# Optimization experiments

Measured on AMD Instinct MI355X. Metric: run time of the kernel, lower is better.

The kernel has to match this reference:

```python
import jax, jax.numpy as jnp
import numpy as np

B, H, OUT, L_LAYERS = 64, 1024, 512, 2
SEQ = 256
SOS_VALUE = -2.0  # predict_binary_output=False


def setup_inputs() -> dict:
    key = jax.random.key(0)
    ks = jax.random.split(key, 16)
    s_ih0 = 1.0 / np.sqrt(OUT)
    s_h = 1.0 / np.sqrt(H)
    return {
        "encoder_output": jax.random.normal(ks[0], (B, SEQ, OUT), jnp.float32),
        "h0": jax.random.normal(ks[1], (L_LAYERS, B, H), jnp.float32),
        "c0": jax.random.normal(ks[2], (L_LAYERS, B, H), jnp.float32),
        "W_ih0": jax.random.normal(ks[3], (4 * H, OUT), jnp.float32) * s_ih0,
        "W_hh0": jax.random.normal(ks[4], (4 * H, H), jnp.float32) * s_h,
        "b_ih0": jax.random.normal(ks[5], (4 * H,), jnp.float32) * s_h,
        "b_hh0": jax.random.normal(ks[6], (4 * H,), jnp.float32) * s_h,
        "W_ih1": jax.random.normal(ks[7], (4 * H, H), jnp.float32) * s_h,
        "W_hh1": jax.random.normal(ks[8], (4 * H, H), jnp.float32) * s_h,
        "b_ih1": jax.random.normal(ks[9], (4 * H,), jnp.float32) * s_h,
        "b_hh1": jax.random.normal(ks[10], (4 * H,), jnp.float32) * s_h,
        "W_fc": jax.random.normal(ks[11], (OUT, H), jnp.float32) * s_h,
        "b_fc": jax.random.normal(ks[12], (OUT,), jnp.float32) * s_h,
        "seq_length": SEQ,
    }


def _lstm_cell(x, h, c, Wih, Whh, bih, bhh):
    # PyTorch gate order: i, f, g, o
    gates = x @ Wih.T + h @ Whh.T + (bih + bhh)
    i, f, g, o = jnp.split(gates, 4, axis=-1)
    i = jax.nn.sigmoid(i)
    f = jax.nn.sigmoid(f)
    g = jnp.tanh(g)
    o = jax.nn.sigmoid(o)
    c_new = f * c + i * g
    h_new = o * jnp.tanh(c_new)
    return h_new, c_new


def reference(encoder_output, h0, c0, W_ih0, W_hh0, b_ih0, b_hh0,
              W_ih1, W_hh1, b_ih1, b_hh1, W_fc, b_fc, seq_length):
    batch = h0.shape[1]
    y_init = jnp.full((batch, OUT), SOS_VALUE, dtype=h0.dtype)  # SOS token
    layers = ((W_ih0, W_hh0, b_ih0, b_hh0), (W_ih1, W_hh1, b_ih1, b_hh1))

    def step(carry, _):
        h, c, y = carry  # h, c: (num_layers, B, H); y: (B, OUT)
        x = y
        hs, cs = [], []
        for l, (Wih, Whh, bih, bhh) in enumerate(layers):
            h_l, c_l = _lstm_cell(x, h[l], c[l], Wih, Whh, bih, bhh)
            hs.append(h_l)
            cs.append(c_l)
            x = h_l
        y_hat = jax.nn.relu(x @ W_fc.T + b_fc)
        return (jnp.stack(hs), jnp.stack(cs), y_hat), y_hat

    (_, _, _), ys = jax.lax.scan(step, (h0, c0, y_init), None, length=seq_length)
    return jnp.transpose(ys, (1, 0, 2))  # (B, seq_length, OUT)
```

## Files before the change

kernel.cpp:

```cpp
#include <hip/hip_runtime.h>
#include <stdint.h>


#define NBLK 256
#define NTHR 256
#define HDIM 1024
#define ODIM 512
#define BDIM 64
#define SEQL 256
#define LEAD0 224

typedef _Float16 v8h __attribute__((ext_vector_type(8)));
typedef float    v4f __attribute__((ext_vector_type(4)));

#define WL0_NS 48
#define WL1_NS 64
#define WFC_NS 32
#define WL0_OFF 0
#define WL1_OFF (WL0_NS*1024)
#define WFC_OFF (WL1_OFF + WL1_NS*1024)
#define SMEM_BYTES (WFC_OFF + WFC_NS*1024)

#define YB_SZ  (BDIM*ODIM*2)
#define HB_SZ  (BDIM*HDIM*2)

#define FH0_REL 0
#define FH1_REL (4*256*4)
#define FY_REL  (FH1_REL + 4*256*4)
#define EH0_REL (FY_REL + 4*32*4)
#define EY_REL  (EH0_REL + 4*8*64)
#define FLG_BYTES (EY_REL + 4*8*64)

__device__ __forceinline__ float fsig(float x)   { return 1.0f / (1.0f + __expf(-x)); }
__device__ __forceinline__ float ftanhf(float x) { return 1.0f - 2.0f / (__expf(2.0f*x) + 1.0f); }

__device__ __forceinline__ unsigned long long ald8(const void* p){
  return __hip_atomic_load((const unsigned long long*)p, __ATOMIC_RELAXED, __HIP_MEMORY_SCOPE_AGENT);
}
__device__ __forceinline__ unsigned int ald4(const void* p){
  return __hip_atomic_load((const unsigned int*)p, __ATOMIC_RELAXED, __HIP_MEMORY_SCOPE_AGENT);
}
__device__ __forceinline__ void ast4(void* p, unsigned int v){
  __hip_atomic_store((unsigned int*)p, v, __ATOMIC_RELAXED, __HIP_MEMORY_SCOPE_AGENT);
}

__device__ __forceinline__ void wrap_inv(){
  asm volatile("s_waitcnt vmcnt(0)\n\tbuffer_inv sc1" ::: "memory");
}

__device__ __forceinline__ void wait_word(const unsigned int* w, unsigned int tag){
  while (ald4(w) < tag) __builtin_amdgcn_s_sleep(1);
  asm volatile("" ::: "memory");
}

__device__ __forceinline__ void scan256_pub(const unsigned int* rowf, unsigned int* ew,
                                            unsigned int tag){
  const char* p = (const char*)(rowf + (threadIdx.x & 63)*4);
  while (true){
    unsigned long long a = ald8(p);
    unsigned long long b = ald8(p+8);
    unsigned int m0 = (unsigned int)a, m1 = (unsigned int)(a >> 32);
    unsigned int m2 = (unsigned int)b, m3 = (unsigned int)(b >> 32);
    unsigned int m = min(min(m0, m1), min(m2, m3));
    if (__all(m >= tag)) break;
    __builtin_amdgcn_s_sleep(1);
  }
  if ((threadIdx.x & 63) == 0) ast4(ew, tag);
  asm volatile("" ::: "memory");
}

__device__ __forceinline__ void scan32_pub(const unsigned int* rowf, unsigned int* ew,
                                           unsigned int tag){
  const unsigned int* p = rowf + (threadIdx.x & 31);
  while (!__all(ald4(p) >= tag)) __builtin_amdgcn_s_sleep(1);
  if ((threadIdx.x & 63) == 0) ast4(ew, tag);
  asm volatile("" ::: "memory");
}

__device__ __forceinline__ void wait_grp256(const unsigned int* rowf, unsigned int tag){
  const char* p = (const char*)(rowf + (threadIdx.x & 63)*4);
  while (true){
    unsigned long long a = ald8(p);
    unsigned long long b = ald8(p+8);
    unsigned int m0 = (unsigned int)a, m1 = (unsigned int)(a >> 32);
    unsigned int m2 = (unsigned int)b, m3 = (unsigned int)(b >> 32);
    unsigned int m = min(min(m0, m1), min(m2, m3));
    if (__all(m >= tag)) break;
    __builtin_amdgcn_s_sleep(1);
  }
  asm volatile("" ::: "memory");
}

__device__ __forceinline__ void publish(unsigned int* flag, unsigned int tag){
  asm volatile("s_waitcnt vmcnt(0)" ::: "memory");
  if ((threadIdx.x & 63) == 0) ast4(flag, tag);
}

template<int NC>
__device__ __forceinline__ v4f gemm_phase(const char* const cb[], const char* wl, v4f acc){
  v8h A[4][8];
  constexpr int PF = (NC < 3) ? NC : 3;
  #pragma unroll
  for (int p = 0; p < PF; p++){
    #pragma unroll
    for (int j = 0; j < 8; j++) A[p][j] = *(const v8h*)(cb[p] + (size_t)j*64);
  }
  #pragma unroll
  for (int c = 0; c < NC; c++){
    const int cur = c & 3, nx = (c + 3) & 3;
    if (c + 3 < NC){
      #pragma unroll
      for (int j = 0; j < 8; j++) A[nx][j] = *(const v8h*)(cb[c+3] + (size_t)j*64);
    }
    #pragma unroll
    for (int j = 0; j < 8; j++){
      v8h B = *(const v8h*)(wl + (size_t)(c*8 + j)*1024);
      acc = __builtin_amdgcn_mfma_f32_16x16x32_f16(A[cur][j], B, acc, 0, 0, 0);
    }
  }
  return acc;
}

__device__ __forceinline__ void gemm_dual4(const char* const cb[], const char* wlA,
                                           const char* wlB, v4f& accA, v4f& accB){
  v8h A[4][8];
  #pragma unroll
  for (int p = 0; p < 3; p++){
    #pragma unroll
    for (int j = 0; j < 8; j++) A[p][j] = *(const v8h*)(cb[p] + (size_t)j*64);
  }
  #pragma unroll
  for (int c = 0; c < 4; c++){
    const int cur = c & 3, nx = (c + 3) & 3;
    if (c + 3 < 4){
      #pragma unroll
      for (int j = 0; j < 8; j++) A[nx][j] = *(const v8h*)(cb[c+3] + (size_t)j*64);
    }
    #pragma unroll
    for (int j = 0; j < 8; j++){
      v8h BA = *(const v8h*)(wlA + (size_t)(c*8 + j)*1024);
      accA = __builtin_amdgcn_mfma_f32_16x16x32_f16(A[cur][j], BA, accA, 0, 0, 0);
      v8h BB = *(const v8h*)(wlB + (size_t)(c*8 + j)*1024);
      accB = __builtin_amdgcn_mfma_f32_16x16x32_f16(A[cur][j], BB, accB, 0, 0, 0);
    }
  }
}

__device__ __forceinline__ void lstm_epi_pack(v4f acc, float bias, float* cs,
                                              char* hbase, int l15, int gidx){
  #pragma unroll
  for (int r = 0; r < 4; r++){
    float v  = acc[r] + bias;
    float x1 = __shfl_xor(v, 1);
    float x2 = __shfl_xor(v, 2);
    float x3 = __shfl_xor(v, 3);
    float vi = (gidx==0)?v :(gidx==1)?x1:(gidx==2)?x2:x3;
    float vf = (gidx==1)?v :(gidx==0)?x1:(gidx==3)?x2:x3;
    float vg = (gidx==2)?v :(gidx==3)?x1:(gidx==0)?x2:x3;
    float vo = (gidx==3)?v :(gidx==2)?x1:(gidx==1)?x2:x3;
    float ii = fsig(vi), ff = fsig(vf), gg = ftanhf(vg), oo = fsig(vo);
    float cn = ff*cs[r] + ii*gg;
    cs[r] = cn;
    float hn = oo * ftanhf(cn);
    unsigned int uv = (unsigned int)__builtin_bit_cast(unsigned short, (_Float16)hn);
    unsigned int o4 = (unsigned int)__shfl_xor((int)uv, 4);
    unsigned int pr = uv | (o4 << 16);
    unsigned int o8 = (unsigned int)__shfl_xor((int)pr, 8);
    if (l15 == 0){
      unsigned long long full = (unsigned long long)pr | ((unsigned long long)o8 << 32);
      __hip_atomic_store((unsigned long long*)(hbase + (size_t)r*(HDIM*2)), full,
                         __ATOMIC_RELAXED, __HIP_MEMORY_SCOPE_AGENT);
    }
  }
}

__global__ void init_kernel(const float* __restrict__ h0,
                            _Float16* __restrict__ h0bi, _Float16* __restrict__ h1bi,
                            _Float16* __restrict__ ybi){
  int i = blockIdx.x*256 + threadIdx.x;
  if (i < BDIM*HDIM){
    h0bi[i] = (_Float16)h0[i];
    h1bi[i] = (_Float16)h0[BDIM*HDIM + i];
  }
  if (i < BDIM*ODIM) ybi[i] = (_Float16)(-2.0f);
}

__launch_bounds__(NTHR, 1)
__global__ void decoder_kernel(
    const float* __restrict__ Wih0, const float* __restrict__ Whh0,
    const float* __restrict__ bih0, const float* __restrict__ bhh0,
    const float* __restrict__ Wih1, const float* __restrict__ Whh1,
    const float* __restrict__ bih1, const float* __restrict__ bhh1,
    const float* __restrict__ Wfc,  const float* __restrict__ bfc,
    const float* __restrict__ c0in, float* __restrict__ out,
    char* __restrict__ yB, char* __restrict__ h0B, char* __restrict__ h1B,
    char* __restrict__ flg, int dmask)
{
  extern __shared__ char smem[];
  const int bid = blockIdx.x;
  const int tid = threadIdx.x;
  const int wv  = tid >> 6;
  const int ln  = tid & 63;
  const int l15 = ln & 15;
  const int lq  = ln >> 4;
  const int u0  = bid * 4;
  const int f   = bid & 7;
  const int leader = (bid >= LEAD0 && bid < LEAD0 + 8);

  unsigned int* fh0r = (unsigned int*)(flg + FH0_REL) + wv*256;
  unsigned int* fh1r = (unsigned int*)(flg + FH1_REL) + wv*256;
  unsigned int* fyr  = (unsigned int*)(flg + FY_REL)  + wv*32;
  unsigned int* eh0  = (unsigned int*)(flg + EH0_REL + (wv*8 + f)*64);
  unsigned int* ey   = (unsigned int*)(flg + EY_REL  + (wv*8 + f)*64);

  for (int slot = tid; slot < WL0_NS*64; slot += NTHR){
    int s = slot >> 6, l = slot & 63;
    int r16 = l & 15, q = l >> 4;
    int grow = (r16 & 3)*HDIM + u0 + (r16 >> 2);
    int kb = s*32 + q*8;
    const float* src; int k0;
    if (kb < ODIM){ src = Wih0 + (size_t)grow*ODIM; k0 = kb; }
    else          { src = Whh0 + (size_t)grow*HDIM; k0 = kb - ODIM; }
    v8h hv;
    #pragma unroll
    for (int j = 0; j < 8; j++) hv[j] = (_Float16)src[k0 + j];
    *(v8h*)(smem + WL0_OFF + s*1024 + l*16) = hv;
  }
  for (int slot = tid; slot < WL1_NS*64; slot += NTHR){
    int s = slot >> 6, l = slot & 63;
    int r16 = l & 15, q = l >> 4;
    int grow = (r16 & 3)*HDIM + u0 + (r16 >> 2);
    int kb = s*32 + q*8;
    const float* src; int k0;
    if (kb < HDIM){ src = Wih1 + (size_t)grow*HDIM; k0 = kb; }
    else          { src = Whh1 + (size_t)grow*HDIM; k0 = kb - HDIM; }
    v8h hv;
    #pragma unroll
    for (int j = 0; j < 8; j++) hv[j] = (_Float16)src[k0 + j];
    *(v8h*)(smem + WL1_OFF + s*1024 + l*16) = hv;
  }
  if (bid < 32){
    for (int slot = tid; slot < WFC_NS*64; slot += NTHR){
      int s = slot >> 6, l = slot & 63;
      int r16 = l & 15, q = l >> 4;
      const float* src = Wfc + (size_t)(bid*16 + r16)*HDIM;
      int k0 = s*32 + q*8;
      v8h hv;
      #pragma unroll
      for (int j = 0; j < 8; j++) hv[j] = (_Float16)src[k0 + j];
      *(v8h*)(smem + WFC_OFF + s*1024 + l*16) = hv;
    }
  }
  __syncthreads();

  const int gidx = l15 & 3;
  const int unit = u0 + (l15 >> 2);
  const int growL = gidx*HDIM + unit;
  const float bias0 = bih0[growL] + bhh0[growL];
  const float bias1 = bih1[growL] + bhh1[growL];
  float biasf = 0.f;
  if (bid < 32) biasf = bfc[bid*16 + l15];

  const int rb = wv*16 + lq*4;
  float cs0[4], cs1[4];
  #pragma unroll
  for (int r = 0; r < 4; r++){
    int b = rb + r;
    cs0[r] = c0in[(size_t)(0*BDIM + b)*HDIM + unit];
    cs1[r] = c0in[(size_t)(1*BDIM + b)*HDIM + unit];
  }

  const int row = wv*16 + l15;
  const size_t aoffY = (size_t)row*ODIM*2 + (size_t)lq*16;
  const size_t aoffH = (size_t)row*HDIM*2 + (size_t)lq*16;
  const size_t hwoff = ((size_t)rb*HDIM + u0)*2;
  const char* wl0 = smem + WL0_OFF + ln*16;
  const char* wl1 = smem + WL1_OFF + ln*16;
  const char* wlf = smem + WFC_OFF + ln*16;
  const char* wl0r = wl0 + 16*1024;
  const char* wl1r = wl1 + 32*1024;

  v4f p0 = {0.f,0.f,0.f,0.f};
  {
    const char* hi = h0B + (size_t)dmask*HB_SZ + aoffH;
    const char* cb[4] = { hi, hi+512, hi+1024, hi+1536 };
    p0 = gemm_phase<4>(cb, wl0r, p0);
  }

  for (int t = 0; t < SEQL; t++){
    const int sp = (t - 1) & dmask;
    const int sc = t & dmask;

    if ((t & dmask) == 0) wrap_inv();

    if (t > 0){
      if (leader) scan32_pub(fyr, ey, (unsigned)t);
      else        wait_word(ey, (unsigned)t);
    }

    {
      const char* ysrc = yB + (size_t)sp*YB_SZ + aoffY;
      const char* cb[2] = { ysrc, ysrc+512 };
      v4f acc = gemm_phase<2>(cb, wl0, p0);
      lstm_epi_pack(acc, bias0, cs0, h0B + (size_t)sc*HB_SZ + hwoff, l15, gidx);
    }
    publish(&fh0r[bid], (unsigned)(t+1));

    v4f p1 = {0.f,0.f,0.f,0.f};
    {
      const char* hs = h1B + (size_t)sp*HB_SZ + aoffH;
      const char* cb[4] = { hs, hs+512, hs+1024, hs+1536 };
      if (leader){
        scan256_pub(fh0r, eh0, (unsigned)(t+1));
        p1 = gemm_phase<4>(cb, wl1r, p1);
      } else {
        p1 = gemm_phase<4>(cb, wl1r, p1);
        wait_word(eh0, (unsigned)(t+1));
      }
    }

    {
      const char* hs = h0B + (size_t)sc*HB_SZ + aoffH;
      const char* cb[4] = { hs, hs+512, hs+1024, hs+1536 };
      v4f np0 = {0.f,0.f,0.f,0.f};
      gemm_dual4(cb, wl1, wl0r, p1, np0);
      lstm_epi_pack(p1, bias1, cs1, h1B + (size_t)sc*HB_SZ + hwoff, l15, gidx);
      p0 = np0;
    }
    publish(&fh1r[bid], (unsigned)(t+1));

    if (bid < 32){
      wait_grp256(fh1r, (unsigned)(t+1));
      const char* f1 = h1B + (size_t)sc*HB_SZ + aoffH;
      const char* cb[4] = { f1, f1+512, f1+1024, f1+1536 };
      v4f acc = {0.f,0.f,0.f,0.f};
      acc = gemm_phase<4>(cb, wlf, acc);
      char* ydst = yB + (size_t)sc*YB_SZ;
      float yv[4];
      #pragma unroll
      for (int r = 0; r < 4; r++){
        float v = fmaxf(acc[r] + biasf, 0.f);
        yv[r] = v;
        unsigned int uv = (unsigned int)__builtin_bit_cast(unsigned short, (_Float16)v);
        unsigned int o1 = (unsigned int)__shfl_xor((int)uv, 1);
        unsigned int pr = uv | (o1 << 16);
        unsigned int o2 = (unsigned int)__shfl_xor((int)pr, 2);
        if ((l15 & 3) == 0){
          int b = rb + r;
          int o = bid*16 + l15;
          unsigned long long full = (unsigned long long)pr | ((unsigned long long)o2 << 32);
          __hip_atomic_store((unsigned long long*)(ydst + ((size_t)b*ODIM + o)*2),
                             full, __ATOMIC_RELAXED, __HIP_MEMORY_SCOPE_AGENT);
        }
      }
      publish(&fyr[bid], (unsigned)(t+1));
      #pragma unroll
      for (int r = 0; r < 4; r++){
        int b = rb + r;
        int o = bid*16 + l15;
        out[((size_t)b*SEQL + t)*ODIM + o] = yv[r];
      }
    }
  }
}

extern "C" void kernel_launch(void* const* d_in, const int* in_sizes, int n_in,
                              void* d_out, int out_size, void* d_ws, size_t ws_size,
                              hipStream_t stream){
  (void)in_sizes; (void)n_in; (void)out_size;

  int D = 16;
  while (D > 2 && (size_t)D*(YB_SZ + 2*HB_SZ) + FLG_BYTES > ws_size) D >>= 1;
  if ((size_t)D*(YB_SZ + 2*HB_SZ) + FLG_BYTES > ws_size) return;

  char* ws  = (char*)d_ws;
  char* yB  = ws;
  char* h0B = yB + (size_t)D*YB_SZ;
  char* h1B = h0B + (size_t)D*HB_SZ;
  char* flg = h1B + (size_t)D*HB_SZ;

  const float* h0   = (const float*)d_in[1];
  const float* c0   = (const float*)d_in[2];
  const float* Wih0 = (const float*)d_in[3];
  const float* Whh0 = (const float*)d_in[4];
  const float* bih0 = (const float*)d_in[5];
  const float* bhh0 = (const float*)d_in[6];
  const float* Wih1 = (const float*)d_in[7];
  const float* Whh1 = (const float*)d_in[8];
  const float* bih1 = (const float*)d_in[9];
  const float* bhh1 = (const float*)d_in[10];
  const float* Wfc  = (const float*)d_in[11];
  const float* bfc  = (const float*)d_in[12];
  float* out = (float*)d_out;

  (void)hipMemsetAsync(flg, 0, FLG_BYTES, stream);
  hipLaunchKernelGGL(init_kernel, dim3(256), dim3(256), 0, stream,
                     h0,
                     (_Float16*)(h0B + (size_t)(D-1)*HB_SZ),
                     (_Float16*)(h1B + (size_t)(D-1)*HB_SZ),
                     (_Float16*)(yB  + (size_t)(D-1)*YB_SZ));

  (void)hipFuncSetAttribute((const void*)decoder_kernel,
                            hipFuncAttributeMaxDynamicSharedMemorySize, SMEM_BYTES);
  hipLaunchKernelGGL(decoder_kernel, dim3(NBLK), dim3(NTHR), SMEM_BYTES, stream,
                     Wih0, Whh0, bih0, bhh0, Wih1, Whh1, bih1, bhh1,
                     Wfc, bfc, c0, out, yB, h0B, h1B, flg, D - 1);
}
```

Measured before the change: 5.753 ms.

## Spread FC output projection across all blocks and split sync leaders per stage

```diff
diff --git a/kernel.cpp b/kernel.cpp
--- a/kernel.cpp
+++ b/kernel.cpp
@@ -8,7 +8,6 @@
 #define ODIM 512
 #define BDIM 64
 #define SEQL 256
-#define LEAD0 224
 
 typedef _Float16 v8h __attribute__((ext_vector_type(8)));
 typedef float    v4f __attribute__((ext_vector_type(4)));
@@ -27,8 +26,9 @@
 #define FH0_REL 0
 #define FH1_REL (4*256*4)
 #define FY_REL  (FH1_REL + 4*256*4)
-#define EH0_REL (FY_REL + 4*32*4)
-#define EY_REL  (EH0_REL + 4*8*64)
+#define EH0_REL (FY_REL + 4*256*4)
+#define EH1_REL (EH0_REL + 4*8*64)
+#define EY_REL  (EH1_REL + 4*8*64)
 #define FLG_BYTES (EY_REL + 4*8*64)
 
 __device__ __forceinline__ float fsig(float x)   { return 1.0f / (1.0f + __expf(-x)); }
@@ -66,28 +66,6 @@
     __builtin_amdgcn_s_sleep(1);
   }
   if ((threadIdx.x & 63) == 0) ast4(ew, tag);
-  asm volatile("" ::: "memory");
-}
-
-__device__ __forceinline__ void scan32_pub(const unsigned int* rowf, unsigned int* ew,
-                                           unsigned int tag){
-  const unsigned int* p = rowf + (threadIdx.x & 31);
-  while (!__all(ald4(p) >= tag)) __builtin_amdgcn_s_sleep(1);
-  if ((threadIdx.x & 63) == 0) ast4(ew, tag);
-  asm volatile("" ::: "memory");
-}
-
-__device__ __forceinline__ void wait_grp256(const unsigned int* rowf, unsigned int tag){
-  const char* p = (const char*)(rowf + (threadIdx.x & 63)*4);
-  while (true){
-    unsigned long long a = ald8(p);
-    unsigned long long b = ald8(p+8);
-    unsigned int m0 = (unsigned int)a, m1 = (unsigned int)(a >> 32);
-    unsigned int m2 = (unsigned int)b, m3 = (unsigned int)(b >> 32);
-    unsigned int m = min(min(m0, m1), min(m2, m3));
-    if (__all(m >= tag)) break;
-    __builtin_amdgcn_s_sleep(1);
-  }
   asm volatile("" ::: "memory");
 }
 
@@ -205,12 +183,15 @@
   const int lq  = ln >> 4;
   const int u0  = bid * 4;
   const int f   = bid & 7;
-  const int leader = (bid >= LEAD0 && bid < LEAD0 + 8);
+  const int lead_h0 = (bid < 8);
+  const int lead_h1 = (bid >= 8  && bid < 16);
+  const int lead_y  = (bid >= 16 && bid < 24);
 
   unsigned int* fh0r = (unsigned int*)(flg + FH0_REL) + wv*256;
   unsigned int* fh1r = (unsigned int*)(flg + FH1_REL) + wv*256;
-  unsigned int* fyr  = (unsigned int*)(flg + FY_REL)  + wv*32;
+  unsigned int* fyr  = (unsigned int*)(flg + FY_REL)  + wv*256;
   unsigned int* eh0  = (unsigned int*)(flg + EH0_REL + (wv*8 + f)*64);
+  unsigned int* eh1  = (unsigned int*)(flg + EH1_REL + (wv*8 + f)*64);
   unsigned int* ey   = (unsigned int*)(flg + EY_REL  + (wv*8 + f)*64);
 
   for (int slot = tid; slot < WL0_NS*64; slot += NTHR){
@@ -239,17 +220,20 @@
     for (int j = 0; j < 8; j++) hv[j] = (_Float16)src[k0 + j];
     *(v8h*)(smem + WL1_OFF + s*1024 + l*16) = hv;
   }
-  if (bid < 32){
-    for (int slot = tid; slot < WFC_NS*64; slot += NTHR){
-      int s = slot >> 6, l = slot & 63;
-      int r16 = l & 15, q = l >> 4;
-      const float* src = Wfc + (size_t)(bid*16 + r16)*HDIM;
-      int k0 = s*32 + q*8;
-      v8h hv;
+  for (int slot = tid; slot < WFC_NS*64; slot += NTHR){
+    int s = slot >> 6, l = slot & 63;
+    int r16 = l & 15, q = l >> 4;
+    int k0 = s*32 + q*8;
+    v8h hv;
+    if (r16 < 2){
+      const float* src = Wfc + (size_t)(bid*2 + r16)*HDIM;
       #pragma unroll
       for (int j = 0; j < 8; j++) hv[j] = (_Float16)src[k0 + j];
-      *(v8h*)(smem + WFC_OFF + s*1024 + l*16) = hv;
-    }
+    } else {
+      #pragma unroll
+      for (int j = 0; j < 8; j++) hv[j] = (_Float16)0.0f;
+    }
+    *(v8h*)(smem + WFC_OFF + s*1024 + l*16) = hv;
   }
   __syncthreads();
 
@@ -258,8 +242,7 @@
   const int growL = gidx*HDIM + unit;
   const float bias0 = bih0[growL] + bhh0[growL];
   const float bias1 = bih1[growL] + bhh1[growL];
-  float biasf = 0.f;
-  if (bid < 32) biasf = bfc[bid*16 + l15];
+  const float biasf = (l15 < 2) ? bfc[bid*2 + l15] : 0.f;
 
   const int rb = wv*16 + lq*4;
   float cs0[4], cs1[4];
@@ -294,7 +277,7 @@
     if ((t & dmask) == 0) wrap_inv();
 
     if (t > 0){
-      if (leader) scan32_pub(fyr, ey, (unsigned)t);
+      if (lead_y) scan256_pub(fyr, ey, (unsigned)t);
       else        wait_word(ey, (unsigned)t);
     }
 
@@ -310,13 +293,9 @@
     {
       const char* hs = h1B + (size_t)sp*HB_SZ + aoffH;
       const char* cb[4] = { hs, hs+512, hs+1024, hs+1536 };
-      if (leader){
-        scan256_pub(fh0r, eh0, (unsigned)(t+1));
-        p1 = gemm_phase<4>(cb, wl1r, p1);
-      } else {
-        p1 = gemm_phase<4>(cb, wl1r, p1);
-        wait_word(eh0, (unsigned)(t+1));
-      }
+      p1 = gemm_phase<4>(cb, wl1r, p1);
+      if (lead_h0) scan256_pub(fh0r, eh0, (unsigned)(t+1));
+      else         wait_word(eh0, (unsigned)(t+1));
     }
 
     {
@@ -329,38 +308,29 @@
     }
     publish(&fh1r[bid], (unsigned)(t+1));
 
-    if (bid < 32){
-      wait_grp256(fh1r, (unsigned)(t+1));
+    if (lead_h1) scan256_pub(fh1r, eh1, (unsigned)(t+1));
+    else         wait_word(eh1, (unsigned)(t+1));
+
+    {
       const char* f1 = h1B + (size_t)sc*HB_SZ + aoffH;
       const char* cb[4] = { f1, f1+512, f1+1024, f1+1536 };
       v4f acc = {0.f,0.f,0.f,0.f};
       acc = gemm_phase<4>(cb, wlf, acc);
       char* ydst = yB + (size_t)sc*YB_SZ;
-      float yv[4];
       #pragma unroll
       for (int r = 0; r < 4; r++){
         float v = fmaxf(acc[r] + biasf, 0.f);
-        yv[r] = v;
+        int b = rb + r;
         unsigned int uv = (unsigned int)__builtin_bit_cast(unsigned short, (_Float16)v);
         unsigned int o1 = (unsigned int)__shfl_xor((int)uv, 1);
-        unsigned int pr = uv | (o1 << 16);
-        unsigned int o2 = (unsigned int)__shfl_xor((int)pr, 2);
-        if ((l15 & 3) == 0){
-          int b = rb + r;
-          int o = bid*16 + l15;
-          unsigned long long full = (unsigned long long)pr | ((unsigned long long)o2 << 32);
-          __hip_atomic_store((unsigned long long*)(ydst + ((size_t)b*ODIM + o)*2),
-                             full, __ATOMIC_RELAXED, __HIP_MEMORY_SCOPE_AGENT);
+        if (l15 == 0){
+          unsigned int pr = uv | (o1 << 16);
+          ast4(ydst + ((size_t)b*ODIM + bid*2)*2, pr);
         }
+        if (l15 < 2) out[((size_t)b*SEQL + t)*ODIM + bid*2 + l15] = v;
       }
-      publish(&fyr[bid], (unsigned)(t+1));
-      #pragma unroll
-      for (int r = 0; r < 4; r++){
-        int b = rb + r;
-        int o = bid*16 + l15;
-        out[((size_t)b*SEQL + t)*ODIM + o] = yv[r];
-      }
-    }
+    }
+    publish(&fyr[bid], (unsigned)(t+1));
   }
 }
 
```

Result: faster. 4.919 ms (median of 2 runs) (-14.5%).
